# Kernel optimization log

Hardware: AMD Instinct MI355X
Metric: run time of the kernel (lower is better)

Reference implementation:

```python
import jax, jax.numpy as jnp
import numpy as np

C = 192; G = 12; CG = C // G          # channels, groups, channels per group
KS = 3; PAD = 1; K = KS * KS - 1      # 3x3 kernel, remove_center=True -> 8 points
HID = 4 * C                           # mlp_ratio = 4
OFFSET_SCALE = 1.0

# kernel dilation grid (x, y) pairs, center removed (remove_center=True)
_pts = np.arange(KS) - (KS - 1) // 2
_gx, _gy = np.meshgrid(_pts, _pts, indexing='ij')
_grid = np.stack([_gx.ravel(), _gy.ravel()], -1).astype(np.float32)
_grid = _grid[~np.all(_grid == 0, axis=1)]   # (K, 2)
GRID = jnp.asarray(_grid)


def _ln(x, w, b, eps=1e-5):
    mu = jnp.mean(x, -1, keepdims=True)
    var = jnp.var(x, -1, keepdims=True)
    return (x - mu) * jax.lax.rsqrt(var + eps) * w + b


def _dcnv3(x, in_proj_w, in_proj_b, dw_w, dw_b, dw_ln_w, dw_ln_b,
           off_w, off_b, mask_w, mask_b, cfs_w, cfs_b, out_proj_w, out_proj_b):
    # x: (B, H, W, C) channels-last
    B, H, W, _ = x.shape
    xp = x @ in_proj_w + in_proj_b          # value / x_proj
    # depthwise conv -> LN -> GELU on the raw input (offset/mask branch)
    x1 = jax.lax.conv_general_dilated(
        x, dw_w, (1, 1), 'SAME',
        dimension_numbers=('NHWC', 'HWIO', 'NHWC'),
        feature_group_count=C) + dw_b
    x1 = jax.nn.gelu(_ln(x1, dw_ln_w, dw_ln_b, 1e-6), approximate=False)
    off = (x1 @ off_w + off_b).reshape(B, H, W, G, K, 2)      # (dx, dy) in pixels
    mask = jax.nn.softmax((x1 @ mask_w + mask_b).reshape(B, H, W, G, K), axis=-1)
    # pad value and flatten spatial; (B, Hp*Wp, G, 1, CG)
    Hp, Wp = H + 2 * PAD, W + 2 * PAD
    v = jnp.pad(xp, ((0, 0), (PAD, PAD), (PAD, PAD), (0, 0))).reshape(B, Hp * Wp, G, 1, CG)
    # sampling locations in padded-image pixel index coords (grid_sample align_corners=False)
    bx = jnp.arange(W, dtype=x.dtype)[None, None, :, None, None] + PAD
    by = jnp.arange(H, dtype=x.dtype)[None, :, None, None, None] + PAD
    px = (bx + (GRID[:, 0] + off[..., 0]) * OFFSET_SCALE).reshape(B, H * W, G, K)
    py = (by + (GRID[:, 1] + off[..., 1]) * OFFSET_SCALE).reshape(B, H * W, G, K)
    x0 = jnp.floor(px); y0 = jnp.floor(py)
    wx = px - x0; wy = py - y0
    ix0 = x0.astype(jnp.int32); iy0 = y0.astype(jnp.int32)

    def gather(iy, ix):
        valid = ((iy >= 0) & (iy < Hp) & (ix >= 0) & (ix < Wp)).astype(x.dtype)
        idx = jnp.clip(iy, 0, Hp - 1) * Wp + jnp.clip(ix, 0, Wp - 1)
        s = jnp.take_along_axis(v, idx[..., None], axis=1)    # (B, HW, G, K, CG)
        return s * valid[..., None]

    s = (gather(iy0, ix0)         * ((1 - wy) * (1 - wx))[..., None]
       + gather(iy0, ix0 + 1)     * ((1 - wy) * wx)[..., None]
       + gather(iy0 + 1, ix0)     * (wy * (1 - wx))[..., None]
       + gather(iy0 + 1, ix0 + 1) * (wy * wx)[..., None])
    out = jnp.einsum('bngk,bngkc->bngc', mask.reshape(B, H * W, G, K), s).reshape(B, H, W, C)
    # center feature scale
    cfs = jax.nn.sigmoid(x1 @ cfs_w.T + cfs_b)                # (B, H, W, G)
    cfs = jnp.repeat(cfs, CG, axis=-1)                        # (B, H, W, C)
    out = out * (1 - cfs) + xp * cfs
    return out @ out_proj_w + out_proj_b


def _forward(x, norm1_w, norm1_b, norm2_w, norm2_b, rpn1_w, rpn1_b, rpn2_w, rpn2_b,
             in_proj_w, in_proj_b, dw_w, dw_b, dw_ln_w, dw_ln_b, off_w, off_b,
             mask_w, mask_b, cfs_w, cfs_b, out_proj_w, out_proj_b,
             fc1_w, fc1_b, fc2_w, fc2_b):
    d = _dcnv3(_ln(x, norm1_w, norm1_b), in_proj_w, in_proj_b, dw_w, dw_b,
               dw_ln_w, dw_ln_b, off_w, off_b, mask_w, mask_b, cfs_w, cfs_b,
               out_proj_w, out_proj_b)
    x = x + _ln(d, rpn1_w, rpn1_b)                            # res_post_norm branch 1
    h = jax.nn.gelu(_ln(x, norm2_w, norm2_b) @ fc1_w + fc1_b, approximate=False) @ fc2_w + fc2_b
    x = x + _ln(h, rpn2_w, rpn2_b)                            # res_post_norm branch 2
    return x


def setup_inputs():
    key = jax.random.key(0)
    ks = jax.random.split(key, 12)
    r = lambda i, shape, s=0.02: jax.random.normal(ks[i], shape, jnp.float32) * s
    B, H, W = 4, 56, 56
    return dict(
        x=jax.random.normal(ks[0], (B, H, W, C), jnp.float32),
        norm1_w=jnp.ones((C,)), norm1_b=jnp.zeros((C,)),
        norm2_w=jnp.ones((C,)), norm2_b=jnp.zeros((C,)),
        rpn1_w=jnp.ones((C,)), rpn1_b=jnp.zeros((C,)),
        rpn2_w=jnp.ones((C,)), rpn2_b=jnp.zeros((C,)),
        in_proj_w=r(1, (C, C)), in_proj_b=jnp.zeros((C,)),
        dw_w=r(2, (KS, KS, 1, C), 0.1), dw_b=jnp.zeros((C,)),
        dw_ln_w=jnp.ones((C,)), dw_ln_b=jnp.zeros((C,)),
        off_w=r(3, (C, G * K * 2), 0.1), off_b=jnp.zeros((G * K * 2,)),
        mask_w=r(4, (C, G * K), 0.1), mask_b=jnp.zeros((G * K,)),
        cfs_w=r(5, (G, C), 0.1), cfs_b=jnp.zeros((G,)),
        out_proj_w=r(6, (C, C)), out_proj_b=jnp.zeros((C,)),
        fc1_w=r(7, (C, HID)), fc1_b=jnp.zeros((HID,)),
        fc2_w=r(8, (HID, C)), fc2_b=jnp.zeros((C,)),
    )


def reference(x, norm1_w, norm1_b, norm2_w, norm2_b, rpn1_w, rpn1_b, rpn2_w, rpn2_b,
              in_proj_w, in_proj_b, dw_w, dw_b, dw_ln_w, dw_ln_b, off_w, off_b,
              mask_w, mask_b, cfs_w, cfs_b, out_proj_w, out_proj_b,
              fc1_w, fc1_b, fc2_w, fc2_b):
    return _forward(x, norm1_w, norm1_b, norm2_w, norm2_b, rpn1_w, rpn1_b, rpn2_w, rpn2_b,
                    in_proj_w, in_proj_b, dw_w, dw_b, dw_ln_w, dw_ln_b, off_w, off_b,
                    mask_w, mask_b, cfs_w, cfs_b, out_proj_w, out_proj_b,
                    fc1_w, fc1_b, fc2_w, fc2_b)
```

## Files before the change

kernel.cpp:

```cpp
#include <hip/hip_runtime.h>
#include <hip/hip_bf16.h>
#include <math.h>


#define BATCH 4
#define HH 56
#define WW 56
#define CC 192
#define NPIX (BATCH * HH * WW)
#define XS_STR 200
#define H1S 776
#define OFS 193
#define MLS 97

typedef __hip_bfloat16 bf16;
typedef __attribute__((ext_vector_type(8))) short short8;
typedef __attribute__((ext_vector_type(4))) float float4v;

__device__ __forceinline__ float gelu_exact(float x) {
    return 0.5f * x * (1.f + erff(x * 0.70710678118654752f));
}
__device__ __forceinline__ bf16 f2b(float f) { return __float2bfloat16(f); }
__device__ __forceinline__ float b2f(bf16 h) { return __bfloat162float(h); }
__device__ __forceinline__ float b2fu(short s) {
    return __uint_as_float((unsigned)(unsigned short)s << 16);
}
__device__ __forceinline__ float4 ldb4(const bf16* p) {
    const ushort4 u = *(const ushort4*)p;
    float4 r;
    r.x = __uint_as_float((unsigned)u.x << 16);
    r.y = __uint_as_float((unsigned)u.y << 16);
    r.z = __uint_as_float((unsigned)u.z << 16);
    r.w = __uint_as_float((unsigned)u.w << 16);
    return r;
}
__device__ __forceinline__ void stb4(bf16* p, float4 v) {
    ushort4 u;
    bf16 h;
    h = f2b(v.x); u.x = *(unsigned short*)&h;
    h = f2b(v.y); u.y = *(unsigned short*)&h;
    h = f2b(v.z); u.z = *(unsigned short*)&h;
    h = f2b(v.w); u.w = *(unsigned short*)&h;
    *(ushort4*)p = u;
}

__global__ __launch_bounds__(256) void prep_w_k(const float* __restrict__ inpw,
        const float* __restrict__ offw, const float* __restrict__ maskw,
        const float* __restrict__ cfsw, const float* __restrict__ outpw,
        const float* __restrict__ fc1w, const float* __restrict__ fc2w,
        bf16* __restrict__ wsB)
{
    const int i = blockIdx.x * 256 + threadIdx.x;
    bf16* inpP = wsB;
    bf16* omP  = wsB + 36864;
    bf16* outP = wsB + 95232;
    bf16* fc1P = wsB + 132096;
    bf16* fc2P = wsB + 279552;
    const int j   = i & 7;
    const int l   = (i >> 3) & 63;
    const int n15 = l & 15, q = l >> 4;
    const int grp = i >> 9;
    if (i < 36864) {
        const int t = grp / 6, c = grp - t * 6;
        const int n = 16 * t + n15, k = 32 * c + 8 * q + j;
        inpP[i] = f2b(inpw[(size_t)k * 192 + n]);
        outP[i] = f2b(outpw[(size_t)k * 192 + n]);
    }
    if (i < 58368) {
        const int t = grp / 6, c = grp - t * 6;
        const int n = 16 * t + n15, k = 32 * c + 8 * q + j;
        omP[i] = (n < 192) ? f2b(offw[(size_t)k * 192 + n])
               : (n < 288) ? f2b(maskw[(size_t)k * 96 + (n - 192)])
               : (n < 300) ? f2b(cfsw[(size_t)(n - 288) * 192 + k])
                           : f2b(0.f);
    }
    if (i < 147456) {
        const int t1 = grp / 6, c1 = grp - t1 * 6;
        const int n1 = 16 * t1 + n15, k1 = 32 * c1 + 8 * q + j;
        fc1P[i] = f2b(fc1w[(size_t)k1 * 768 + n1]);
        const int t2 = grp / 24, c2 = grp - t2 * 24;
        const int n2 = 16 * t2 + n15, k2 = 32 * c2 + 8 * q + j;
        fc2P[i] = f2b(fc2w[(size_t)k2 * 192 + n2]);
    }
}

__global__ __launch_bounds__(256) void ln_gemm16_k(const float* __restrict__ x,
        const float* __restrict__ n1w, const float* __restrict__ n1b,
        const bf16* __restrict__ wP, const float* __restrict__ bias,
        bf16* __restrict__ xn_out, bf16* __restrict__ xp_out)
{
    __shared__ __align__(16) bf16 xs[16 * XS_STR];
    const int tid = threadIdx.x;
    const int w   = tid >> 6;
    const int l   = tid & 63;
    const int n15 = l & 15;
    const int q   = l >> 4;
    const int p0  = blockIdx.x * 16;

    #pragma unroll
    for (int rr = 0; rr < 4; rr++) {
        const int lr = 4 * w + rr;
        const size_t base = (size_t)(p0 + lr) * CC;
        float v[3];
        #pragma unroll
        for (int i = 0; i < 3; i++) v[i] = x[base + l + 64 * i];
        float s = v[0] + v[1] + v[2];
        float qq = v[0]*v[0] + v[1]*v[1] + v[2]*v[2];
        #pragma unroll
        for (int off = 32; off > 0; off >>= 1) {
            s  += __shfl_xor(s, off, 64);
            qq += __shfl_xor(qq, off, 64);
        }
        const float mu  = s * (1.f / CC);
        const float var = qq * (1.f / CC) - mu * mu;
        const float rs  = rsqrtf(var + 1e-5f);
        #pragma unroll
        for (int i = 0; i < 3; i++) {
            const int c = l + 64 * i;
            const bf16 h = f2b((v[i] - mu) * rs * n1w[c] + n1b[c]);
            xs[lr * XS_STR + c] = h;
            xn_out[base + c] = h;
        }
    }
    __syncthreads();

    short8 aF[6];
    #pragma unroll
    for (int c = 0; c < 6; c++)
        aF[c] = *(const short8*)&xs[n15 * XS_STR + c * 32 + q * 8];

    #pragma unroll
    for (int t = 0; t < 3; t++) {
        const int tile = 3 * w + t;
        float4v acc = (float4v){0.f, 0.f, 0.f, 0.f};
        #pragma unroll
        for (int c = 0; c < 6; c++) {
            const short8 bF = *(const short8*)&wP[(size_t)((tile * 6 + c) * 64 + l) * 8];
            acc = __builtin_amdgcn_mfma_f32_16x16x32_bf16(aF[c], bF, acc, 0, 0, 0);
        }
        const int n0 = 16 * tile;
        const float bb = bias[n0 + n15];
        #pragma unroll
        for (int r = 0; r < 4; r++)
            xp_out[(size_t)(p0 + 4 * q + r) * 192 + n0 + n15] = f2b(acc[r] + bb);
    }
}

__global__ __launch_bounds__(256) void offmask_sample_k(
        const bf16* __restrict__ xp, const bf16* __restrict__ xn,
        const float* __restrict__ dww, const float* __restrict__ dwb,
        const float* __restrict__ dwlnw, const float* __restrict__ dwlnb,
        const bf16* __restrict__ omP, const float* __restrict__ offb,
        const float* __restrict__ maskb, const float* __restrict__ cfsb,
        bf16* __restrict__ outb)
{
    __shared__ __align__(16) bf16 xs[8 * XS_STR];
    __shared__ float cv[8][192];
    __shared__ float offs_l[8][OFS];
    __shared__ float mls_l[8][MLS];
    __shared__ float cfs_l[8][16];

    const int tid = threadIdx.x;
    const int w   = tid >> 6;
    const int l   = tid & 63;
    const int n15 = l & 15;
    const int q   = l >> 4;
    const int bid = (blockIdx.x & 7) * (NPIX / 64) + (blockIdx.x >> 3);
    const int p0  = bid * 8;

    const int bimg = p0 / (HH * WW);
    const int rem  = p0 - bimg * HH * WW;
    const int h    = rem / WW;
    const int wx0  = rem - h * WW;

    #pragma unroll
    for (int pass = 0; pass < 2; pass++) {
        const int px = w + 4 * pass;
        if (l < 48) {
            const int c0 = l * 4;
            const int wx = wx0 + px;
            float4 acc = *(const float4*)&dwb[c0];
            #pragma unroll
            for (int ky = 0; ky < 3; ky++) {
                const int yy = h + ky - 1;
                if (yy < 0 || yy >= HH) continue;
                #pragma unroll
                for (int kx = 0; kx < 3; kx++) {
                    const int xx = wx + kx - 1;
                    if (xx < 0 || xx >= WW) continue;
                    const float4 a = ldb4(&xn[((size_t)(bimg * HH + yy) * WW + xx) * CC + c0]);
                    const float4 ww = *(const float4*)&dww[(ky * 3 + kx) * CC + c0];
                    acc.x += a.x * ww.x; acc.y += a.y * ww.y;
                    acc.z += a.z * ww.z; acc.w += a.w * ww.w;
                }
            }
            *(float4*)&cv[px][c0] = acc;
        }
    }
    __syncthreads();

    #pragma unroll
    for (int pass = 0; pass < 2; pass++) {
        const int px = w + 4 * pass;
        float v[3];
        #pragma unroll
        for (int i = 0; i < 3; i++) v[i] = cv[px][l + 64 * i];
        float s = v[0] + v[1] + v[2];
        float qq = v[0]*v[0] + v[1]*v[1] + v[2]*v[2];
        #pragma unroll
        for (int off = 32; off > 0; off >>= 1) {
            s  += __shfl_xor(s, off, 64);
            qq += __shfl_xor(qq, off, 64);
        }
        const float mu  = s * (1.f / CC);
        const float var = qq * (1.f / CC) - mu * mu;
        const float rs  = rsqrtf(var + 1e-6f);
        #pragma unroll
        for (int i = 0; i < 3; i++) {
            const int c = l + 64 * i;
            xs[px * XS_STR + c] = f2b(gelu_exact((v[i] - mu) * rs * dwlnw[c] + dwlnb[c]));
        }
    }
    __syncthreads();

    {
        short8 aF[6];
        #pragma unroll
        for (int c = 0; c < 6; c++)
            aF[c] = (n15 < 8)
                  ? *(const short8*)&xs[n15 * XS_STR + c * 32 + q * 8]
                  : (short8){0, 0, 0, 0, 0, 0, 0, 0};

        for (int t = w; t < 19; t += 4) {
            float4v acc = (float4v){0.f, 0.f, 0.f, 0.f};
            #pragma unroll
            for (int c = 0; c < 6; c++) {
                const short8 bF = *(const short8*)&omP[(size_t)((t * 6 + c) * 64 + l) * 8];
                acc = __builtin_amdgcn_mfma_f32_16x16x32_bf16(aF[c], bF, acc, 0, 0, 0);
            }
            if (t < 12) {
                const int n0 = 16 * t;
                const float bb = offb[n0 + n15];
                if (q < 2) {
                    #pragma unroll
                    for (int r = 0; r < 4; r++)
                        offs_l[4 * q + r][n0 + n15] = acc[r] + bb;
                }
            } else if (t < 18) {
                const int m0 = 16 * t - 192;
                const float bb = maskb[m0 + n15];
                #pragma unroll
                for (int r = 0; r < 4; r++) {
                    const float vv = acc[r] + bb;
                    float mx = vv;
                    mx = fmaxf(mx, __shfl_xor(mx, 1, 64));
                    mx = fmaxf(mx, __shfl_xor(mx, 2, 64));
                    mx = fmaxf(mx, __shfl_xor(mx, 4, 64));
                    const float e = expf(vv - mx);
                    float se = e;
                    se += __shfl_xor(se, 1, 64);
                    se += __shfl_xor(se, 2, 64);
                    se += __shfl_xor(se, 4, 64);
                    if (q < 2) mls_l[4 * q + r][m0 + n15] = e * (1.f / se);
                }
            } else {
                const float bb = (n15 < 12) ? cfsb[n15] : 0.f;
                #pragma unroll
                for (int r = 0; r < 4; r++) {
                    const float cf = 1.f / (1.f + expf(-(acc[r] + bb)));
                    if (q < 2 && n15 < 12) cfs_l[4 * q + r][n15] = cf;
                }
            }
        }
    }
    __syncthreads();

    if (tid < 192) {
        const int px  = tid / 24;
        const int s2  = tid - px * 24;
        const int g   = s2 >> 1;
        const int ch0 = g * 16 + (s2 & 1) * 8;
        const int pix = p0 + px;
        const int wxp = wx0 + px;

        float mk[8];
        #pragma unroll
        for (int k = 0; k < 8; k++) mk[k] = mls_l[px][g * 8 + k];
        const float cf = cfs_l[px][g];

        const int GX[8] = {-1, -1, -1, 0, 0, 1, 1, 1};
        const int GY[8] = {-1, 0, 1, -1, 1, -1, 0, 1};
        const size_t imgbase = (size_t)bimg * HH * WW * CC;

        float acc[8];
        #pragma unroll
        for (int j = 0; j < 8; j++) acc[j] = 0.f;

        #pragma unroll 2
        for (int k = 0; k < 8; k++) {
            const float px_ = (float)wxp + (float)GX[k] + offs_l[px][g * 16 + 2 * k];
            const float py_ = (float)h   + (float)GY[k] + offs_l[px][g * 16 + 2 * k + 1];
            const float fx = floorf(px_), fy = floorf(py_);
            const float wxf = px_ - fx, wyf = py_ - fy;
            const int x0 = (int)fx, y0 = (int)fy;
            const short8 z8 = {0, 0, 0, 0, 0, 0, 0, 0};
            short8 v00 = z8, v01 = z8, v10 = z8, v11 = z8;
            const bool xin0 = (x0 >= 0) && (x0 < WW);
            const bool xin1 = (x0 + 1 >= 0) && (x0 + 1 < WW);
            if (y0 >= 0 && y0 < HH) {
                if (xin0) v00 = *(const short8*)&xp[imgbase + (size_t)(y0 * WW + x0) * CC + ch0];
                if (xin1) v01 = *(const short8*)&xp[imgbase + (size_t)(y0 * WW + x0 + 1) * CC + ch0];
            }
            if (y0 + 1 >= 0 && y0 + 1 < HH) {
                if (xin0) v10 = *(const short8*)&xp[imgbase + (size_t)((y0 + 1) * WW + x0) * CC + ch0];
                if (xin1) v11 = *(const short8*)&xp[imgbase + (size_t)((y0 + 1) * WW + x0 + 1) * CC + ch0];
            }
            const float w00 = mk[k] * (1.f - wyf) * (1.f - wxf);
            const float w01 = mk[k] * (1.f - wyf) * wxf;
            const float w10 = mk[k] * wyf * (1.f - wxf);
            const float w11 = mk[k] * wyf * wxf;
            #pragma unroll
            for (int j = 0; j < 8; j++) {
                acc[j] += w00 * b2fu(v00[j]) + w01 * b2fu(v01[j])
                        + w10 * b2fu(v10[j]) + w11 * b2fu(v11[j]);
            }
        }

        const short8 xv = *(const short8*)&xp[(size_t)pix * CC + ch0];
        short8 o;
        #pragma unroll
        for (int j = 0; j < 8; j++) {
            const float ov = acc[j] * (1.f - cf) + b2fu(xv[j]) * cf;
            bf16 hh = f2b(ov);
            o[j] = *(short*)&hh;
        }
        *(short8*)&outb[(size_t)pix * CC + ch0] = o;
    }
}

__global__ __launch_bounds__(256) void gemm_ln2_mlp_k(const bf16* __restrict__ A,
        const bf16* __restrict__ wP, const float* __restrict__ bias,
        const float* __restrict__ x,
        const float* __restrict__ r1w, const float* __restrict__ r1b,
        const float* __restrict__ n2w, const float* __restrict__ n2b,
        const bf16* __restrict__ fc1P, const float* __restrict__ fc1b,
        const bf16* __restrict__ fc2P, const float* __restrict__ fc2b,
        const float* __restrict__ r2w, const float* __restrict__ r2b,
        float* __restrict__ out)
{
    __shared__ __align__(16) bf16 xs[16 * XS_STR];
    __shared__ __align__(16) bf16 h1[16 * H1S];
    __shared__ float ps[4][16], pq[4][16], ps2[4][16], pq2[4][16];

    const int tid = threadIdx.x;
    const int w   = tid >> 6;
    const int l   = tid & 63;
    const int n15 = l & 15;
    const int q   = l >> 4;
    const int p0  = blockIdx.x * 16;

    for (int i = tid; i < 16 * 24; i += 256) {
        const int px = i / 24, c8 = i - px * 24;
        *(short8*)&xs[px * XS_STR + c8 * 8] = *(const short8*)&A[(size_t)(p0 + px) * 192 + c8 * 8];
    }
    __syncthreads();

    {
        short8 aF[6];
        #pragma unroll
        for (int c = 0; c < 6; c++)
            aF[c] = *(const short8*)&xs[n15 * XS_STR + c * 32 + q * 8];

        float4v acc[3];
        #pragma unroll
        for (int t = 0; t < 3; t++) {
            const int tile = 3 * w + t;
            acc[t] = (float4v){0.f, 0.f, 0.f, 0.f};
            #pragma unroll
            for (int c = 0; c < 6; c++) {
                const short8 bF = *(const short8*)&wP[(size_t)((tile * 6 + c) * 64 + l) * 8];
                acc[t] = __builtin_amdgcn_mfma_f32_16x16x32_bf16(aF[c], bF, acc[t], 0, 0, 0);
            }
            const float bb = bias[16 * tile + n15];
            #pragma unroll
            for (int r = 0; r < 4; r++) acc[t][r] += bb;
        }

        #pragma unroll
        for (int r = 0; r < 4; r++) {
            float sp = acc[0][r] + acc[1][r] + acc[2][r];
            float qp = acc[0][r]*acc[0][r] + acc[1][r]*acc[1][r] + acc[2][r]*acc[2][r];
            #pragma unroll
            for (int o = 1; o < 16; o <<= 1) {
                sp += __shfl_xor(sp, o, 64);
                qp += __shfl_xor(qp, o, 64);
            }
            if (n15 == 0) { ps[w][4 * q + r] = sp; pq[w][4 * q + r] = qp; }
        }
        __syncthreads();

        float x2v[3][4];
        #pragma unroll
        for (int r = 0; r < 4; r++) {
            const int row = 4 * q + r;
            const float s  = ps[0][row] + ps[1][row] + ps[2][row] + ps[3][row];
            const float qq = pq[0][row] + pq[1][row] + pq[2][row] + pq[3][row];
            const float mu  = s * (1.f / CC);
            const float var = qq * (1.f / CC) - mu * mu;
            const float rs  = rsqrtf(var + 1e-5f);
            const size_t grow = p0 + row;
            #pragma unroll
            for (int t = 0; t < 3; t++) {
                const int col = 48 * w + 16 * t + n15;
                x2v[t][r] = x[grow * CC + col] + (acc[t][r] - mu) * rs * r1w[col] + r1b[col];
            }
        }
        #pragma unroll
        for (int r = 0; r < 4; r++) {
            float sp = x2v[0][r] + x2v[1][r] + x2v[2][r];
            float qp = x2v[0][r]*x2v[0][r] + x2v[1][r]*x2v[1][r] + x2v[2][r]*x2v[2][r];
            #pragma unroll
            for (int o = 1; o < 16; o <<= 1) {
                sp += __shfl_xor(sp, o, 64);
                qp += __shfl_xor(qp, o, 64);
            }
            if (n15 == 0) { ps2[w][4 * q + r] = sp; pq2[w][4 * q + r] = qp; }
        }
        __syncthreads();

        #pragma unroll
        for (int r = 0; r < 4; r++) {
            const int row = 4 * q + r;
            const float s  = ps2[0][row] + ps2[1][row] + ps2[2][row] + ps2[3][row];
            const float qq = pq2[0][row] + pq2[1][row] + pq2[2][row] + pq2[3][row];
            const float mu  = s * (1.f / CC);
            const float var = qq * (1.f / CC) - mu * mu;
            const float rs  = rsqrtf(var + 1e-5f);
            #pragma unroll
            for (int t = 0; t < 3; t++) {
                const int col = 48 * w + 16 * t + n15;
                xs[row * XS_STR + col] = f2b((x2v[t][r] - mu) * rs * n2w[col] + n2b[col]);
            }
        }
        __syncthreads();

        short8 aF2[6];
        #pragma unroll
        for (int c = 0; c < 6; c++)
            aF2[c] = *(const short8*)&xs[n15 * XS_STR + c * 32 + q * 8];

        #pragma unroll
        for (int t1 = 0; t1 < 12; t1++) {
            const int tile = 12 * w + t1;
            float4v a1 = (float4v){0.f, 0.f, 0.f, 0.f};
            #pragma unroll
            for (int c = 0; c < 6; c++) {
                const short8 bF = *(const short8*)&fc1P[(size_t)((tile * 6 + c) * 64 + l) * 8];
                a1 = __builtin_amdgcn_mfma_f32_16x16x32_bf16(aF2[c], bF, a1, 0, 0, 0);
            }
            const int n0 = 16 * tile;
            const float bb = fc1b[n0 + n15];
            #pragma unroll
            for (int r = 0; r < 4; r++)
                h1[(4 * q + r) * H1S + n0 + n15] = f2b(gelu_exact(a1[r] + bb));
        }
        __syncthreads();

        float4v acc2[3];
        #pragma unroll
        for (int t = 0; t < 3; t++) acc2[t] = (float4v){0.f, 0.f, 0.f, 0.f};
        #pragma unroll 4
        for (int kc = 0; kc < 24; kc++) {
            const short8 a2 = *(const short8*)&h1[n15 * H1S + kc * 32 + q * 8];
            #pragma unroll
            for (int t = 0; t < 3; t++) {
                const int tile = 3 * w + t;
                const short8 bF = *(const short8*)&fc2P[(size_t)((tile * 24 + kc) * 64 + l) * 8];
                acc2[t] = __builtin_amdgcn_mfma_f32_16x16x32_bf16(a2, bF, acc2[t], 0, 0, 0);
            }
        }
        #pragma unroll
        for (int t = 0; t < 3; t++) {
            const float bb = fc2b[48 * w + 16 * t + n15];
            #pragma unroll
            for (int r = 0; r < 4; r++) acc2[t][r] += bb;
        }

        #pragma unroll
        for (int r = 0; r < 4; r++) {
            float sp = acc2[0][r] + acc2[1][r] + acc2[2][r];
            float qp = acc2[0][r]*acc2[0][r] + acc2[1][r]*acc2[1][r] + acc2[2][r]*acc2[2][r];
            #pragma unroll
            for (int o = 1; o < 16; o <<= 1) {
                sp += __shfl_xor(sp, o, 64);
                qp += __shfl_xor(qp, o, 64);
            }
            if (n15 == 0) { ps[w][4 * q + r] = sp; pq[w][4 * q + r] = qp; }
        }
        __syncthreads();

        #pragma unroll
        for (int r = 0; r < 4; r++) {
            const int row = 4 * q + r;
            const float s  = ps[0][row] + ps[1][row] + ps[2][row] + ps[3][row];
            const float qq = pq[0][row] + pq[1][row] + pq[2][row] + pq[3][row];
            const float mu  = s * (1.f / CC);
            const float var = qq * (1.f / CC) - mu * mu;
            const float rs  = rsqrtf(var + 1e-5f);
            const size_t grow = p0 + row;
            #pragma unroll
            for (int t = 0; t < 3; t++) {
                const int col = 48 * w + 16 * t + n15;
                out[grow * CC + col] = x2v[t][r]
                                     + (acc2[t][r] - mu) * rs * r2w[col] + r2b[col];
            }
        }
    }
}

extern "C" void kernel_launch(void* const* d_in, const int* in_sizes, int n_in,
                              void* d_out, int out_size, void* d_ws, size_t ws_size,
                              hipStream_t stream) {
    const float* x      = (const float*)d_in[0];
    const float* n1w    = (const float*)d_in[1];
    const float* n1b    = (const float*)d_in[2];
    const float* n2w    = (const float*)d_in[3];
    const float* n2b    = (const float*)d_in[4];
    const float* rpn1w  = (const float*)d_in[5];
    const float* rpn1b  = (const float*)d_in[6];
    const float* rpn2w  = (const float*)d_in[7];
    const float* rpn2b  = (const float*)d_in[8];
    const float* inpw   = (const float*)d_in[9];
    const float* inpb   = (const float*)d_in[10];
    const float* dww    = (const float*)d_in[11];
    const float* dwb    = (const float*)d_in[12];
    const float* dwlnw  = (const float*)d_in[13];
    const float* dwlnb  = (const float*)d_in[14];
    const float* offw   = (const float*)d_in[15];
    const float* offb   = (const float*)d_in[16];
    const float* maskw  = (const float*)d_in[17];
    const float* maskb  = (const float*)d_in[18];
    const float* cfsw   = (const float*)d_in[19];
    const float* cfsb   = (const float*)d_in[20];
    const float* outpw  = (const float*)d_in[21];
    const float* outpb  = (const float*)d_in[22];
    const float* fc1w   = (const float*)d_in[23];
    const float* fc1b   = (const float*)d_in[24];
    const float* fc2w   = (const float*)d_in[25];
    const float* fc2b   = (const float*)d_in[26];

    const int N = NPIX;
    const size_t NP = (size_t)N * CC;
    bf16* B0  = (bf16*)d_ws;
    bf16* B1  = B0 + NP;
    bf16* B3  = B1 + NP;
    bf16* wsB = B3 + NP;
    const bf16* inpP = wsB;
    const bf16* omP  = wsB + 36864;
    const bf16* outP = wsB + 95232;
    const bf16* fc1P = wsB + 132096;
    const bf16* fc2P = wsB + 279552;

    const int g16 = N / 16;
    const int g8  = N / 8;

    prep_w_k<<<576, 256, 0, stream>>>(inpw, offw, maskw, cfsw, outpw, fc1w, fc2w, wsB);
    ln_gemm16_k<<<g16, 256, 0, stream>>>(x, n1w, n1b, inpP, inpb, B0, B1);
    offmask_sample_k<<<g8, 256, 0, stream>>>(B1, B0, dww, dwb, dwlnw, dwlnb,
                                             omP, offb, maskb, cfsb, B3);
    gemm_ln2_mlp_k<<<g16, 256, 0, stream>>>(B3, outP, outpb, x, rpn1w, rpn1b,
                                            n2w, n2b, fc1P, fc1b, fc2P, fc2b,
                                            rpn2w, rpn2b, (float*)d_out);
}
```

Measured before the change: 192.1 us.

## Fuse offset/mask sampling kernel with output projection and MLP kernel

```diff
diff --git a/kernel.cpp b/kernel.cpp
--- a/kernel.cpp
+++ b/kernel.cpp
@@ -21,27 +21,8 @@
     return 0.5f * x * (1.f + erff(x * 0.70710678118654752f));
 }
 __device__ __forceinline__ bf16 f2b(float f) { return __float2bfloat16(f); }
-__device__ __forceinline__ float b2f(bf16 h) { return __bfloat162float(h); }
 __device__ __forceinline__ float b2fu(short s) {
     return __uint_as_float((unsigned)(unsigned short)s << 16);
-}
-__device__ __forceinline__ float4 ldb4(const bf16* p) {
-    const ushort4 u = *(const ushort4*)p;
-    float4 r;
-    r.x = __uint_as_float((unsigned)u.x << 16);
-    r.y = __uint_as_float((unsigned)u.y << 16);
-    r.z = __uint_as_float((unsigned)u.z << 16);
-    r.w = __uint_as_float((unsigned)u.w << 16);
-    return r;
-}
-__device__ __forceinline__ void stb4(bf16* p, float4 v) {
-    ushort4 u;
-    bf16 h;
-    h = f2b(v.x); u.x = *(unsigned short*)&h;
-    h = f2b(v.y); u.y = *(unsigned short*)&h;
-    h = f2b(v.z); u.z = *(unsigned short*)&h;
-    h = f2b(v.w); u.w = *(unsigned short*)&h;
-    *(ushort4*)p = u;
 }
 
 __global__ __launch_bounds__(256) void prep_w_k(const float* __restrict__ inpw,
@@ -146,40 +127,55 @@
     }
 }
 
-__global__ __launch_bounds__(256) void offmask_sample_k(
+__global__ __launch_bounds__(256) void sample_mlp_k(
         const bf16* __restrict__ xp, const bf16* __restrict__ xn,
         const float* __restrict__ dww, const float* __restrict__ dwb,
         const float* __restrict__ dwlnw, const float* __restrict__ dwlnb,
         const bf16* __restrict__ omP, const float* __restrict__ offb,
         const float* __restrict__ maskb, const float* __restrict__ cfsb,
-        bf16* __restrict__ outb)
+        const bf16* __restrict__ wP, const float* __restrict__ bias,
+        const float* __restrict__ x,
+        const float* __restrict__ r1w, const float* __restrict__ r1b,
+        const float* __restrict__ n2w, const float* __restrict__ n2b,
+        const bf16* __restrict__ fc1P, const float* __restrict__ fc1b,
+        const bf16* __restrict__ fc2P, const float* __restrict__ fc2b,
+        const float* __restrict__ r2w, const float* __restrict__ r2b,
+        float* __restrict__ out)
 {
-    __shared__ __align__(16) bf16 xs[8 * XS_STR];
-    __shared__ float cv[8][192];
-    __shared__ float offs_l[8][OFS];
-    __shared__ float mls_l[8][MLS];
-    __shared__ float cfs_l[8][16];
+    __shared__ __align__(16) bf16 xs[16 * XS_STR];
+    __shared__ __align__(16) char uni[16 * H1S * 2];
+    __shared__ float ps[4][16], pq[4][16], ps2[4][16], pq2[4][16];
+
+    float (*cv)[192]     = (float(*)[192])uni;
+    float (*offs_l)[OFS] = (float(*)[OFS])uni;
+    float (*mls_l)[MLS]  = (float(*)[MLS])(uni + 12352);
+    float (*cfs_l)[16]   = (float(*)[16])(uni + 18560);
+    bf16* h1             = (bf16*)uni;
 
     const int tid = threadIdx.x;
     const int w   = tid >> 6;
     const int l   = tid & 63;
     const int n15 = l & 15;
     const int q   = l >> 4;
-    const int bid = (blockIdx.x & 7) * (NPIX / 64) + (blockIdx.x >> 3);
-    const int p0  = bid * 8;
-
-    const int bimg = p0 / (HH * WW);
-    const int rem  = p0 - bimg * HH * WW;
-    const int h    = rem / WW;
-    const int wx0  = rem - h * WW;
+    const int bid = (blockIdx.x & 7) * (NPIX / 128) + (blockIdx.x >> 3);
+    const int p0  = bid * 16;
 
     #pragma unroll
-    for (int pass = 0; pass < 2; pass++) {
-        const int px = w + 4 * pass;
-        if (l < 48) {
-            const int c0 = l * 4;
-            const int wx = wx0 + px;
-            float4 acc = *(const float4*)&dwb[c0];
+    for (int it = 0; it < 2; it++) {
+        const int id = tid + 256 * it;
+        if (id < 384) {
+            const int px  = id / 24, c8 = id - px * 24;
+            const int ch0 = c8 * 8;
+            const int pix = p0 + px;
+            const int bimg = pix / (HH * WW);
+            const int hw   = pix - bimg * (HH * WW);
+            const int h    = hw / WW;
+            const int wx   = hw - h * WW;
+            float a[8];
+            const float4 bb0 = *(const float4*)&dwb[ch0];
+            const float4 bb1 = *(const float4*)&dwb[ch0 + 4];
+            a[0]=bb0.x; a[1]=bb0.y; a[2]=bb0.z; a[3]=bb0.w;
+            a[4]=bb1.x; a[5]=bb1.y; a[6]=bb1.z; a[7]=bb1.w;
             #pragma unroll
             for (int ky = 0; ky < 3; ky++) {
                 const int yy = h + ky - 1;
@@ -188,19 +184,23 @@
                 for (int kx = 0; kx < 3; kx++) {
                     const int xx = wx + kx - 1;
                     if (xx < 0 || xx >= WW) continue;
-                    const float4 a = ldb4(&xn[((size_t)(bimg * HH + yy) * WW + xx) * CC + c0]);
-                    const float4 ww = *(const float4*)&dww[(ky * 3 + kx) * CC + c0];
-                    acc.x += a.x * ww.x; acc.y += a.y * ww.y;
-                    acc.z += a.z * ww.z; acc.w += a.w * ww.w;
+                    const short8 v = *(const short8*)&xn[((size_t)(bimg * HH + yy) * WW + xx) * CC + ch0];
+                    const float4 w0 = *(const float4*)&dww[(ky * 3 + kx) * CC + ch0];
+                    const float4 w1 = *(const float4*)&dww[(ky * 3 + kx) * CC + ch0 + 4];
+                    a[0] += b2fu(v[0]) * w0.x; a[1] += b2fu(v[1]) * w0.y;
+                    a[2] += b2fu(v[2]) * w0.z; a[3] += b2fu(v[3]) * w0.w;
+                    a[4] += b2fu(v[4]) * w1.x; a[5] += b2fu(v[5]) * w1.y;
+                    a[6] += b2fu(v[6]) * w1.z; a[7] += b2fu(v[7]) * w1.w;
                 }
             }
-            *(float4*)&cv[px][c0] = acc;
+            *(float4*)&cv[px][ch0]     = (float4){a[0], a[1], a[2], a[3]};
+            *(float4*)&cv[px][ch0 + 4] = (float4){a[4], a[5], a[6], a[7]};
         }
     }
     __syncthreads();
 
     #pragma unroll
-    for (int pass = 0; pass < 2; pass++) {
+    for (int pass = 0; pass < 4; pass++) {
         const int px = w + 4 * pass;
         float v[3];
         #pragma unroll
@@ -227,9 +227,7 @@
         short8 aF[6];
         #pragma unroll
         for (int c = 0; c < 6; c++)
-            aF[c] = (n15 < 8)
-                  ? *(const short8*)&xs[n15 * XS_STR + c * 32 + q * 8]
-                  : (short8){0, 0, 0, 0, 0, 0, 0, 0};
+            aF[c] = *(const short8*)&xs[n15 * XS_STR + c * 32 + q * 8];
 
         for (int t = w; t < 19; t += 4) {
             float4v acc = (float4v){0.f, 0.f, 0.f, 0.f};
@@ -241,11 +239,9 @@
             if (t < 12) {
                 const int n0 = 16 * t;
                 const float bb = offb[n0 + n15];
-                if (q < 2) {
-                    #pragma unroll
-                    for (int r = 0; r < 4; r++)
-                        offs_l[4 * q + r][n0 + n15] = acc[r] + bb;
-                }
+                #pragma unroll
+                for (int r = 0; r < 4; r++)
+                    offs_l[4 * q + r][n0 + n15] = acc[r] + bb;
             } else if (t < 18) {
                 const int m0 = 16 * t - 192;
                 const float bb = maskb[m0 + n15];
@@ -261,107 +257,87 @@
                     se += __shfl_xor(se, 1, 64);
                     se += __shfl_xor(se, 2, 64);
                     se += __shfl_xor(se, 4, 64);
-                    if (q < 2) mls_l[4 * q + r][m0 + n15] = e * (1.f / se);
+                    mls_l[4 * q + r][m0 + n15] = e * (1.f / se);
                 }
             } else {
                 const float bb = (n15 < 12) ? cfsb[n15] : 0.f;
                 #pragma unroll
                 for (int r = 0; r < 4; r++) {
                     const float cf = 1.f / (1.f + expf(-(acc[r] + bb)));
-                    if (q < 2 && n15 < 12) cfs_l[4 * q + r][n15] = cf;
+                    if (n15 < 12) cfs_l[4 * q + r][n15] = cf;
                 }
             }
         }
     }
     __syncthreads();
 
-    if (tid < 192) {
-        const int px  = tid / 24;
-        const int s2  = tid - px * 24;
-        const int g   = s2 >> 1;
-        const int ch0 = g * 16 + (s2 & 1) * 8;
-        const int pix = p0 + px;
-        const int wxp = wx0 + px;
-
-        float mk[8];
-        #pragma unroll
-        for (int k = 0; k < 8; k++) mk[k] = mls_l[px][g * 8 + k];
-        const float cf = cfs_l[px][g];
-
-        const int GX[8] = {-1, -1, -1, 0, 0, 1, 1, 1};
-        const int GY[8] = {-1, 0, 1, -1, 1, -1, 0, 1};
-        const size_t imgbase = (size_t)bimg * HH * WW * CC;
-
-        float acc[8];
-        #pragma unroll
-        for (int j = 0; j < 8; j++) acc[j] = 0.f;
-
-        #pragma unroll 2
-        for (int k = 0; k < 8; k++) {
-            const float px_ = (float)wxp + (float)GX[k] + offs_l[px][g * 16 + 2 * k];
-            const float py_ = (float)h   + (float)GY[k] + offs_l[px][g * 16 + 2 * k + 1];
-            const float fx = floorf(px_), fy = floorf(py_);
-            const float wxf = px_ - fx, wyf = py_ - fy;
-            const int x0 = (int)fx, y0 = (int)fy;
-            const short8 z8 = {0, 0, 0, 0, 0, 0, 0, 0};
-            short8 v00 = z8, v01 = z8, v10 = z8, v11 = z8;
-            const bool xin0 = (x0 >= 0) && (x0 < WW);
-            const bool xin1 = (x0 + 1 >= 0) && (x0 + 1 < WW);
-            if (y0 >= 0 && y0 < HH) {
-                if (xin0) v00 = *(const short8*)&xp[imgbase + (size_t)(y0 * WW + x0) * CC + ch0];
-                if (xin1) v01 = *(const short8*)&xp[imgbase + (size_t)(y0 * WW + x0 + 1) * CC + ch0];
-            }
-            if (y0 + 1 >= 0 && y0 + 1 < HH) {
-                if (xin0) v10 = *(const short8*)&xp[imgbase + (size_t)((y0 + 1) * WW + x0) * CC + ch0];
-                if (xin1) v11 = *(const short8*)&xp[imgbase + (size_t)((y0 + 1) * WW + x0 + 1) * CC + ch0];
-            }
-            const float w00 = mk[k] * (1.f - wyf) * (1.f - wxf);
-            const float w01 = mk[k] * (1.f - wyf) * wxf;
-            const float w10 = mk[k] * wyf * (1.f - wxf);
-            const float w11 = mk[k] * wyf * wxf;
+    #pragma unroll
+    for (int it = 0; it < 2; it++) {
+        const int id = tid + 256 * it;
+        if (id < 384) {
+            const int px  = id / 24;
+            const int s2  = id - px * 24;
+            const int g   = s2 >> 1;
+            const int ch0 = g * 16 + (s2 & 1) * 8;
+            const int pix = p0 + px;
+            const int bimg = pix / (HH * WW);
+            const int hw   = pix - bimg * (HH * WW);
+            const int h    = hw / WW;
+            const int wxp  = hw - h * WW;
+
+            float mk[8];
+            #pragma unroll
+            for (int k = 0; k < 8; k++) mk[k] = mls_l[px][g * 8 + k];
+            const float cf = cfs_l[px][g];
+
+            const int GX[8] = {-1, -1, -1, 0, 0, 1, 1, 1};
+            const int GY[8] = {-1, 0, 1, -1, 1, -1, 0, 1};
+            const size_t imgbase = (size_t)bimg * HH * WW * CC;
+
+            float acc[8];
+            #pragma unroll
+            for (int j = 0; j < 8; j++) acc[j] = 0.f;
+
+            #pragma unroll 2
+            for (int k = 0; k < 8; k++) {
+                const float px_ = (float)wxp + (float)GX[k] + offs_l[px][g * 16 + 2 * k];
+                const float py_ = (float)h   + (float)GY[k] + offs_l[px][g * 16 + 2 * k + 1];
+                const float fx = floorf(px_), fy = floorf(py_);
+                const float wxf = px_ - fx, wyf = py_ - fy;
+                const int x0 = (int)fx, y0 = (int)fy;
+                const short8 z8 = {0, 0, 0, 0, 0, 0, 0, 0};
+                short8 v00 = z8, v01 = z8, v10 = z8, v11 = z8;
+                const bool xin0 = (x0 >= 0) && (x0 < WW);
+                const bool xin1 = (x0 + 1 >= 0) && (x0 + 1 < WW);
+                if (y0 >= 0 && y0 < HH) {
+                    if (xin0) v00 = *(const short8*)&xp[imgbase + (size_t)(y0 * WW + x0) * CC + ch0];
+                    if (xin1) v01 = *(const short8*)&xp[imgbase + (size_t)(y0 * WW + x0 + 1) * CC + ch0];
+                }
+                if (y0 + 1 >= 0 && y0 + 1 < HH) {
+                    if (xin0) v10 = *(const short8*)&xp[imgbase + (size_t)((y0 + 1) * WW + x0) * CC + ch0];
+                    if (xin1) v11 = *(const short8*)&xp[imgbase + (size_t)((y0 + 1) * WW + x0 + 1) * CC + ch0];
+                }
+                const float w00 = mk[k] * (1.f - wyf) * (1.f - wxf);
+                const float w01 = mk[k] * (1.f - wyf) * wxf;
+                const float w10 = mk[k] * wyf * (1.f - wxf);
+                const float w11 = mk[k] * wyf * wxf;
+                #pragma unroll
+                for (int j = 0; j < 8; j++) {
+                    acc[j] += w00 * b2fu(v00[j]) + w01 * b2fu(v01[j])
+                            + w10 * b2fu(v10[j]) + w11 * b2fu(v11[j]);
+                }
+            }
+
+            const short8 xv = *(const short8*)&xp[(size_t)pix * CC + ch0];
+            short8 o;
             #pragma unroll
             for (int j = 0; j < 8; j++) {
-                acc[j] += w00 * b2fu(v00[j]) + w01 * b2fu(v01[j])
-                        + w10 * b2fu(v10[j]) + w11 * b2fu(v11[j]);
-            }
-        }
-
-        const short8 xv = *(const short8*)&xp[(size_t)pix * CC + ch0];
-        short8 o;
-        #pragma unroll
-        for (int j = 0; j < 8; j++) {
-            const float ov = acc[j] * (1.f - cf) + b2fu(xv[j]) * cf;
-            bf16 hh = f2b(ov);
-            o[j] = *(short*)&hh;
-        }
-        *(short8*)&outb[(size_t)pix * CC + ch0] = o;
-    }
-}
-
-__global__ __launch_bounds__(256) void gemm_ln2_mlp_k(const bf16* __restrict__ A,
-        const bf16* __restrict__ wP, const float* __restrict__ bias,
-        const float* __restrict__ x,
-        const float* __restrict__ r1w, const float* __restrict__ r1b,
-        const float* __restrict__ n2w, const float* __restrict__ n2b,
-        const bf16* __restrict__ fc1P, const float* __restrict__ fc1b,
-        const bf16* __restrict__ fc2P, const float* __restrict__ fc2b,
-        const float* __restrict__ r2w, const float* __restrict__ r2b,
-        float* __restrict__ out)
-{
-    __shared__ __align__(16) bf16 xs[16 * XS_STR];
-    __shared__ __align__(16) bf16 h1[16 * H1S];
-    __shared__ float ps[4][16], pq[4][16], ps2[4][16], pq2[4][16];
-
-    const int tid = threadIdx.x;
-    const int w   = tid >> 6;
-    const int l   = tid & 63;
-    const int n15 = l & 15;
-    const int q   = l >> 4;
-    const int p0  = blockIdx.x * 16;
-
-    for (int i = tid; i < 16 * 24; i += 256) {
-        const int px = i / 24, c8 = i - px * 24;
-        *(short8*)&xs[px * XS_STR + c8 * 8] = *(const short8*)&A[(size_t)(p0 + px) * 192 + c8 * 8];
+                const float ov = acc[j] * (1.f - cf) + b2fu(xv[j]) * cf;
+                bf16 hh = f2b(ov);
+                o[j] = *(short*)&hh;
+            }
+            *(short8*)&xs[px * XS_STR + ch0] = o;
+        }
     }
     __syncthreads();
 
@@ -553,8 +529,7 @@
     const size_t NP = (size_t)N * CC;
     bf16* B0  = (bf16*)d_ws;
     bf16* B1  = B0 + NP;
-    bf16* B3  = B1 + NP;
-    bf16* wsB = B3 + NP;
+    bf16* wsB = B1 + NP;
     const bf16* inpP = wsB;
     const bf16* omP  = wsB + 36864;
     const bf16* outP = wsB + 95232;
@@ -562,13 +537,12 @@
     const bf16* fc2P = wsB + 279552;
 
     const int g16 = N / 16;
-    const int g8  = N / 8;
 
     prep_w_k<<<576, 256, 0, stream>>>(inpw, offw, maskw, cfsw, outpw, fc1w, fc2w, wsB);
     ln_gemm16_k<<<g16, 256, 0, stream>>>(x, n1w, n1b, inpP, inpb, B0, B1);
-    offmask_sample_k<<<g8, 256, 0, stream>>>(B1, B0, dww, dwb, dwlnw, dwlnb,
-                                             omP, offb, maskb, cfsb, B3);
-    gemm_ln2_mlp_k<<<g16, 256, 0, stream>>>(B3, outP, outpb, x, rpn1w, rpn1b,
-                                            n2w, n2b, fc1P, fc1b, fc2P, fc2b,
-                                            rpn2w, rpn2b, (float*)d_out);
+    sample_mlp_k<<<g16, 256, 0, stream>>>(B1, B0, dww, dwb, dwlnw, dwlnb,
+                                          omP, offb, maskb, cfsb,
+                                          outP, outpb, x, rpn1w, rpn1b,
+                                          n2w, n2b, fc1P, fc1b, fc2P, fc2b,
+                                          rpn2w, rpn2b, (float*)d_out);
 }
```

New measurement: 180.8 us. 1.06x faster.
